# Kernel tuning notes

Measured on AMD Instinct MI355X. Metric: run time of the kernel, lower is better.

Reference implementation:

```python
import jax, jax.numpy as jnp
import numpy as np
import math

B, L, N, DIM, H = 2, 8, 1024, 512, 8
DH = DIM // H

def setup_inputs() -> dict:
    key = jax.random.key(0)
    ks = jax.random.split(key, 9)
    s = 1.0 / math.sqrt(DIM)
    return {
        "x": jax.random.normal(ks[0], (B, L, N, DIM), dtype=jnp.float32),
        "Wq": jax.random.normal(ks[1], (DIM, DIM), dtype=jnp.float32) * s,
        "bq": jnp.zeros((DIM,), dtype=jnp.float32),
        "Wk": jax.random.normal(ks[2], (DIM, DIM), dtype=jnp.float32) * s,
        "bk": jnp.zeros((DIM,), dtype=jnp.float32),
        "Wv": jax.random.normal(ks[3], (DIM, DIM), dtype=jnp.float32) * s,
        "bv": jnp.zeros((DIM,), dtype=jnp.float32),
        "Wo": jax.random.normal(ks[4], (DIM, DIM), dtype=jnp.float32) * s,
        "bo": jnp.zeros((DIM,), dtype=jnp.float32),
    }

def _split_heads(t):
    # 'b l n (h d) -> b l h n d'
    b, l, n, _ = t.shape
    return t.reshape(b, l, n, H, DH).transpose(0, 1, 3, 2, 4)

def reference(x, Wq, bq, Wk, bk, Wv, bv, Wo, bo):
    q = _split_heads(x @ Wq.T + bq)
    # FAITHFUL BUG: source maps (q, v, k) -> (q_mat, k_mat, v_mat),
    # so the "keys" come from the v projection and "values" from the k projection.
    k_mat = _split_heads(x @ Wv.T + bv)
    v_mat = _split_heads(x @ Wk.T + bk)
    # scale is sqrt(Dh * num_heads) = sqrt(dim), as in the source
    scores = jnp.einsum('blhnd,blhmd->blhnm', q, k_mat) / math.sqrt(DIM)
    weights = jax.nn.softmax(scores, axis=-1)
    inter = jnp.einsum('blhnm,blhmd->blhnd', weights, v_mat)
    # 'b l h n d -> b l n (h d)'
    inter = inter.transpose(0, 1, 3, 2, 4).reshape(x.shape[0], x.shape[1], x.shape[2], DIM)
    return inter @ Wo.T + bo
```

## Files before the change

### kernel.cpp

```cpp
#include <hip/hip_runtime.h>
#include <stdint.h>

#define DIMC 512
#define NSEQ 1024
#define BLT  16
#define NHEAD 8
#define DHD  64
#define MTOT (BLT*NSEQ)

typedef float f32x4 __attribute__((ext_vector_type(4)));
typedef short s16x8 __attribute__((ext_vector_type(8)));
typedef short s16x4 __attribute__((ext_vector_type(4)));

__device__ __forceinline__ unsigned short f2bf(float f) {
    unsigned int u = __float_as_uint(f);
    u += 0x7fffu + ((u >> 16) & 1u);
    return (unsigned short)(u >> 16);
}
__device__ __forceinline__ float bf2f(unsigned short h) {
    return __uint_as_float(((unsigned int)h) << 16);
}

#define QSCALE (0.04419417382415922f * 1.4426950408889634f)

__device__ __forceinline__ void gll16(const void* g, void* l) {
    __builtin_amdgcn_global_load_lds(
        (const __attribute__((address_space(1))) void*)g,
        (__attribute__((address_space(3))) void*)l, 16, 0, 0);
}

__device__ __forceinline__ f32x4 mfma16_bf16(s16x4 a, s16x4 b, f32x4 c) {
#if __has_builtin(__builtin_amdgcn_mfma_f32_16x16x16bf16_1k)
    return __builtin_amdgcn_mfma_f32_16x16x16bf16_1k(a, b, c, 0, 0, 0);
#else
    asm volatile("v_mfma_f32_16x16x16_bf16 %0, %1, %2, %0"
                 : "+v"(c) : "v"(a), "v"(b));
    return c;
#endif
}

__device__ __forceinline__ bool detect_bf16(const unsigned short* x) {
    int t = threadIdx.x & 63;
    unsigned short v = x[2 * t];
    int e = (v >> 7) & 0xFF;
    unsigned long long ball = __ballot(e < 100 || e > 137);
    return __popcll(ball) < 16;
}

struct ConvArgs {
    const void* src[9];
    unsigned short* dst[9];
};

__global__ __launch_bounds__(256) void conv_kernel(ConvArgs a,
                                                   const unsigned short* __restrict__ xdet) {
    const bool isbf = detect_bf16(xdet);
    int b = blockIdx.x;
    int seg, idx;
    if (b < 4096)      { seg = 0; idx = (b * 256 + threadIdx.x) * 8; }
    else if (b < 4608) { int t = b - 4096; seg = 1 + (t >> 7);
                         idx = (((t & 127) * 256) + threadIdx.x) * 8; }
    else               { int i = threadIdx.x * 8; seg = 5 + (i >> 9); idx = i & 511; }
    const void* s = a.src[seg];
    unsigned short* d = a.dst[seg];
    if (isbf) {
        *(uint4*)(d + idx) = *(const uint4*)((const unsigned short*)s + idx);
    } else {
        float4 t0 = *(const float4*)((const float*)s + idx);
        float4 t1 = *(const float4*)((const float*)s + idx + 4);
        ushort4 v0{f2bf(t0.x), f2bf(t0.y), f2bf(t0.z), f2bf(t0.w)};
        ushort4 v1{f2bf(t1.x), f2bf(t1.y), f2bf(t1.z), f2bf(t1.w)};
        *(ushort4*)(d + idx)     = v0;
        *(ushort4*)(d + idx + 4) = v1;
    }
}

__device__ __forceinline__ void gemm_core_async(
    const unsigned short* __restrict__ Ap, const unsigned short* __restrict__ Wp,
    int mBase, int nBase, unsigned short* Al, unsigned short* Bl, f32x4 acc[4][4])
{
    const int wave = threadIdx.x >> 6;
    const int lane = threadIdx.x & 63;
    const int lr = lane & 15, lg = lane >> 4;
    const int wm = wave >> 1, wn = wave & 1;
    const int srow = lane >> 3;
    const int scol = (lane & 7) * 8;

    #pragma unroll
    for (int a = 0; a < 4; ++a)
        #pragma unroll
        for (int b = 0; b < 4; ++b) acc[a][b] = (f32x4){0.f, 0.f, 0.f, 0.f};

    for (int k0 = 0; k0 < DIMC; k0 += 64) {
        #pragma unroll
        for (int i = 0; i < 4; ++i) {
            int rbase = (wave * 4 + i) * 8;
            gll16(Ap + (long)(mBase + rbase + srow) * DIMC + k0 + scol, Al + rbase * 64);
            gll16(Wp + (long)(nBase + rbase + srow) * DIMC + k0 + scol, Bl + rbase * 64);
        }
        __syncthreads();

        #pragma unroll
        for (int kk = 0; kk < 64; kk += 32) {
            s16x8 af[4], bf_[4];
            #pragma unroll
            for (int a = 0; a < 4; ++a)
                af[a] = *(const s16x8*)&Al[(wm * 64 + a * 16 + lr) * 64 + kk + lg * 8];
            #pragma unroll
            for (int b = 0; b < 4; ++b)
                bf_[b] = *(const s16x8*)&Bl[(wn * 64 + b * 16 + lr) * 64 + kk + lg * 8];
            #pragma unroll
            for (int a = 0; a < 4; ++a)
                #pragma unroll
                for (int b = 0; b < 4; ++b)
                    acc[a][b] = __builtin_amdgcn_mfma_f32_16x16x32_bf16(af[a], bf_[b], acc[a][b], 0, 0, 0);
        }
        __syncthreads();
    }
}

__global__ __launch_bounds__(256) void proj_kernel(
    const unsigned short* __restrict__ xb,
    const unsigned short* __restrict__ Wqb, const unsigned short* __restrict__ Wkb,
    const unsigned short* __restrict__ Wvb,
    const unsigned short* __restrict__ bqb, const unsigned short* __restrict__ bkb,
    const unsigned short* __restrict__ bvb,
    unsigned short* __restrict__ Q, unsigned short* __restrict__ K,
    unsigned short* __restrict__ Vt)
{
    const int z = blockIdx.z;
    const unsigned short* Wp = (z == 0) ? Wqb : ((z == 1) ? Wvb : Wkb);
    const unsigned short* bp = (z == 0) ? bqb : ((z == 1) ? bvb : bkb);
    unsigned short* outp = (z == 0) ? Q : ((z == 1) ? K : Vt);
    const float oscale = (z == 0) ? QSCALE : 1.0f;

    const int mBase = blockIdx.x * 128;
    const int nBase = blockIdx.y * 128;
    const int lane = threadIdx.x & 63;
    const int lr = lane & 15, lg = lane >> 4;
    const int wm = (threadIdx.x >> 6) >> 1, wn = (threadIdx.x >> 6) & 1;

    __shared__ unsigned short Al[128 * 64];
    __shared__ unsigned short Bl[128 * 64];
    f32x4 acc[4][4];
    gemm_core_async(xb, Wp, mBase, nBase, Al, Bl, acc);

    #pragma unroll
    for (int b = 0; b < 4; ++b) {
        int j = nBase + wn * 64 + b * 16 + lr;
        float bb = bf2f(bp[j]);
        int h = j >> 6, d = j & 63;
        #pragma unroll
        for (int a = 0; a < 4; ++a) {
            int m0 = mBase + wm * 64 + a * 16 + lg * 4;
            int bl = m0 >> 10, n0 = m0 & 1023;
            if (z == 2) {
                ushort4 pk;
                unsigned short* p = (unsigned short*)&pk;
                #pragma unroll
                for (int r = 0; r < 4; ++r) p[r] = f2bf(acc[a][b][r] + bb);
                *(ushort4*)&outp[(((bl << 3) + h) << 16) + (d << 10) + n0] = pk;
            } else {
                #pragma unroll
                for (int r = 0; r < 4; ++r) {
                    float v = (acc[a][b][r] + bb) * oscale;
                    outp[(((bl << 3) + h) << 16) + ((n0 + r) << 6) + d] = f2bf(v);
                }
            }
        }
    }
}

__global__ __launch_bounds__(256) void out_gemm_kernel(
    const unsigned short* __restrict__ inter, const unsigned short* __restrict__ Wob,
    const unsigned short* __restrict__ bob, void* __restrict__ outp,
    const unsigned short* __restrict__ xdet)
{
    const bool isbf = detect_bf16(xdet);
    const int mBase = blockIdx.x * 128;
    const int nBase = blockIdx.y * 128;
    const int lane = threadIdx.x & 63;
    const int lr = lane & 15, lg = lane >> 4;
    const int wm = (threadIdx.x >> 6) >> 1, wn = (threadIdx.x >> 6) & 1;

    __shared__ unsigned short Al[128 * 64];
    __shared__ unsigned short Bl[128 * 64];
    f32x4 acc[4][4];
    gemm_core_async(inter, Wob, mBase, nBase, Al, Bl, acc);

    #pragma unroll
    for (int b = 0; b < 4; ++b) {
        int j = nBase + wn * 64 + b * 16 + lr;
        float bb = bf2f(bob[j]);
        #pragma unroll
        for (int a = 0; a < 4; ++a) {
            #pragma unroll
            for (int r = 0; r < 4; ++r) {
                long m = mBase + wm * 64 + a * 16 + lg * 4 + r;
                float v = acc[a][b][r] + bb;
                if (isbf) ((unsigned short*)outp)[m * DIMC + j] = f2bf(v);
                else      ((float*)outp)[m * DIMC + j] = v;
            }
        }
    }
}

#define SWZ(row, col) ((row) * 64 + ((col) ^ (((row) & 7) * 8)))

__global__ __launch_bounds__(256) void attn_kernel(
    const unsigned short* __restrict__ Q, const unsigned short* __restrict__ K,
    const unsigned short* __restrict__ Vt, unsigned short* __restrict__ inter)
{
    const int inst = blockIdx.x;
    const int bh = inst >> 4;
    const int qt = inst & 15;
    const int wave = threadIdx.x >> 6;
    const int lane = threadIdx.x & 63;
    const int lr = lane & 15;
    const int lg = lane >> 4;

    const unsigned short* Qb = Q + (long)bh * (NSEQ * DHD);
    const int qrow = qt * 64 + wave * 16 + lr;
    s16x8 qf0 = *(const s16x8*)&Qb[qrow * DHD + lg * 8];
    s16x8 qf1 = *(const s16x8*)&Qb[qrow * DHD + 32 + lg * 8];

    __shared__ unsigned short Kl[64 * 64];
    __shared__ unsigned short Vl[64 * 64];

    f32x4 o[4];
    #pragma unroll
    for (int m = 0; m < 4; ++m) o[m] = (f32x4){0.f, 0.f, 0.f, 0.f};
    float l_acc = 0.f;

    for (int kt = 0; kt < 16; ++kt) {
        const unsigned short* Kb = K + (long)bh * (NSEQ * DHD) + kt * 64 * DHD;
        const unsigned short* Vb = Vt + (long)bh * (NSEQ * DHD) + kt * 64;

        #pragma unroll
        for (int i = 0; i < 2; ++i) {
            int f = threadIdx.x + 256 * i;
            int row = f >> 3, c8 = (f & 7) * 8;
            *(uint4*)&Kl[SWZ(row, c8)] = *(const uint4*)&Kb[row * DHD + c8];
            *(uint4*)&Vl[SWZ(row, c8)] = *(const uint4*)&Vb[row * NSEQ + c8];
        }
        __syncthreads();

        f32x4 s[4];
        #pragma unroll
        for (int c = 0; c < 4; ++c) s[c] = (f32x4){0.f, 0.f, 0.f, 0.f};
        #pragma unroll
        for (int kk = 0; kk < 2; ++kk) {
            s16x8 qf = kk ? qf1 : qf0;
            #pragma unroll
            for (int c = 0; c < 4; ++c) {
                s16x8 a = *(const s16x8*)&Kl[SWZ(c * 16 + lr, kk * 32 + lg * 8)];
                s[c] = __builtin_amdgcn_mfma_f32_16x16x32_bf16(a, qf, s[c], 0, 0, 0);
            }
        }

        s16x4 pb[4];
        #pragma unroll
        for (int c = 0; c < 4; ++c) {
            float p0 = __builtin_exp2f(s[c][0]);
            float p1 = __builtin_exp2f(s[c][1]);
            float p2 = __builtin_exp2f(s[c][2]);
            float p3 = __builtin_exp2f(s[c][3]);
            l_acc += (p0 + p1) + (p2 + p3);
            unsigned int u0 = __float_as_uint(p0) + 0x8000u;
            unsigned int u1 = __float_as_uint(p1) + 0x8000u;
            unsigned int u2 = __float_as_uint(p2) + 0x8000u;
            unsigned int u3 = __float_as_uint(p3) + 0x8000u;
            union { s16x4 v; unsigned int u[2]; } pk;
            pk.u[0] = __builtin_amdgcn_perm(u1, u0, 0x07060302u);
            pk.u[1] = __builtin_amdgcn_perm(u3, u2, 0x07060302u);
            pb[c] = pk.v;
        }

        #pragma unroll
        for (int c = 0; c < 4; ++c)
            #pragma unroll
            for (int m = 0; m < 4; ++m) {
                s16x4 a = *(const s16x4*)&Vl[SWZ(m * 16 + lr, c * 16 + lg * 4)];
                o[m] = mfma16_bf16(a, pb[c], o[m]);
            }
        __syncthreads();
    }

    l_acc += __shfl_xor(l_acc, 16);
    l_acc += __shfl_xor(l_acc, 32);
    float inv = 1.f / l_acc;

    const int bl = bh >> 3, h = bh & 7;
    const int n = qt * 64 + wave * 16 + lr;
    #pragma unroll
    for (int m = 0; m < 4; ++m) {
        ushort4 pk;
        unsigned short* p = (unsigned short*)&pk;
        #pragma unroll
        for (int r = 0; r < 4; ++r) p[r] = f2bf(o[m][r] * inv);
        *(ushort4*)&inter[((long)(bl * NSEQ + n)) * DIMC + h * 64 + m * 16 + lg * 4] = pk;
    }
}

extern "C" void kernel_launch(void* const* d_in, const int* in_sizes, int n_in,
                              void* d_out, int out_size, void* d_ws, size_t ws_size,
                              hipStream_t stream) {
    const void* x  = d_in[0];
    const void* Wq = d_in[1]; const void* bq = d_in[2];
    const void* Wk = d_in[3]; const void* bk = d_in[4];
    const void* Wv = d_in[5]; const void* bv = d_in[6];
    const void* Wo = d_in[7]; const void* bo = d_in[8];

    char* ws = (char*)d_ws;
    unsigned short* xb  = (unsigned short*)ws;
    unsigned short* Q   = xb + (long)MTOT * DIMC;
    unsigned short* K   = Q  + (long)MTOT * DIMC;
    unsigned short* Vt  = K  + (long)MTOT * DIMC;
    unsigned short* Wqb = Vt + (long)MTOT * DIMC;
    unsigned short* Wkb = Wqb + DIMC * DIMC;
    unsigned short* Wvb = Wkb + DIMC * DIMC;
    unsigned short* Wob = Wvb + DIMC * DIMC;
    unsigned short* bqb = Wob + DIMC * DIMC;
    unsigned short* bkb = bqb + DIMC;
    unsigned short* bvb = bkb + DIMC;
    unsigned short* bob = bvb + DIMC;

    ConvArgs ca;
    ca.src[0] = x;  ca.src[1] = Wq; ca.src[2] = Wk; ca.src[3] = Wv; ca.src[4] = Wo;
    ca.src[5] = bq; ca.src[6] = bk; ca.src[7] = bv; ca.src[8] = bo;
    ca.dst[0] = xb;  ca.dst[1] = Wqb; ca.dst[2] = Wkb; ca.dst[3] = Wvb; ca.dst[4] = Wob;
    ca.dst[5] = bqb; ca.dst[6] = bkb; ca.dst[7] = bvb; ca.dst[8] = bob;
    conv_kernel<<<4609, 256, 0, stream>>>(ca, (const unsigned short*)x);

    dim3 gp(MTOT / 128, DIMC / 128, 3);
    proj_kernel<<<gp, 256, 0, stream>>>(xb, Wqb, Wkb, Wvb, bqb, bkb, bvb, Q, K, Vt);

    attn_kernel<<<BLT * NHEAD * 16, 256, 0, stream>>>(Q, K, Vt, xb );

    dim3 go(MTOT / 128, DIMC / 128);
    out_gemm_kernel<<<go, 256, 0, stream>>>(xb , Wob, bob, d_out,
                                            (const unsigned short*)x);
}
```

Measured before the change: 248.4 us.

## Process four query tiles per wave in attention to reuse K/V tiles

Each attention block now covers 256 query rows instead of 64. Each wave holds four 16-row query groups and reuses every K and V fragment read from shared memory across all four groups. This cuts global K/V loads and LDS reads per query by a factor of four, and the grid shrinks from 2048 to 512 blocks. In exchange, register pressure rises sharply (64 accumulator vectors plus 64 score vectors per thread), which may lower occupancy or cause spills, and fewer blocks may underfill the GPU.

```diff
diff --git a/kernel.cpp b/kernel.cpp
--- a/kernel.cpp
+++ b/kernel.cpp
@@ -212,25 +212,32 @@
     const unsigned short* __restrict__ Vt, unsigned short* __restrict__ inter)
 {
     const int inst = blockIdx.x;
-    const int bh = inst >> 4;
-    const int qt = inst & 15;
+    const int bh = inst >> 2;
+    const int qt = inst & 3;
     const int wave = threadIdx.x >> 6;
     const int lane = threadIdx.x & 63;
     const int lr = lane & 15;
     const int lg = lane >> 4;
 
     const unsigned short* Qb = Q + (long)bh * (NSEQ * DHD);
-    const int qrow = qt * 64 + wave * 16 + lr;
-    s16x8 qf0 = *(const s16x8*)&Qb[qrow * DHD + lg * 8];
-    s16x8 qf1 = *(const s16x8*)&Qb[qrow * DHD + 32 + lg * 8];
+    const int qbase = qt * 256 + wave * 64;
+
+    s16x8 qf[4][2];
+    #pragma unroll
+    for (int g = 0; g < 4; ++g)
+        #pragma unroll
+        for (int kk = 0; kk < 2; ++kk)
+            qf[g][kk] = *(const s16x8*)&Qb[(qbase + g * 16 + lr) * DHD + kk * 32 + lg * 8];
 
     __shared__ unsigned short Kl[64 * 64];
     __shared__ unsigned short Vl[64 * 64];
 
-    f32x4 o[4];
-    #pragma unroll
-    for (int m = 0; m < 4; ++m) o[m] = (f32x4){0.f, 0.f, 0.f, 0.f};
-    float l_acc = 0.f;
+    f32x4 o[4][4];
+    #pragma unroll
+    for (int g = 0; g < 4; ++g)
+        #pragma unroll
+        for (int m = 0; m < 4; ++m) o[g][m] = (f32x4){0.f, 0.f, 0.f, 0.f};
+    float l_acc[4] = {0.f, 0.f, 0.f, 0.f};
 
     for (int kt = 0; kt < 16; ++kt) {
         const unsigned short* Kb = K + (long)bh * (NSEQ * DHD) + kt * 64 * DHD;
@@ -245,60 +252,75 @@
         }
         __syncthreads();
 
-        f32x4 s[4];
-        #pragma unroll
-        for (int c = 0; c < 4; ++c) s[c] = (f32x4){0.f, 0.f, 0.f, 0.f};
+        f32x4 s[4][4];
+        #pragma unroll
+        for (int g = 0; g < 4; ++g)
+            #pragma unroll
+            for (int c = 0; c < 4; ++c) s[g][c] = (f32x4){0.f, 0.f, 0.f, 0.f};
         #pragma unroll
         for (int kk = 0; kk < 2; ++kk) {
-            s16x8 qf = kk ? qf1 : qf0;
+            s16x8 af[4];
+            #pragma unroll
+            for (int c = 0; c < 4; ++c)
+                af[c] = *(const s16x8*)&Kl[SWZ(c * 16 + lr, kk * 32 + lg * 8)];
+            #pragma unroll
+            for (int g = 0; g < 4; ++g)
+                #pragma unroll
+                for (int c = 0; c < 4; ++c)
+                    s[g][c] = __builtin_amdgcn_mfma_f32_16x16x32_bf16(af[c], qf[g][kk], s[g][c], 0, 0, 0);
+        }
+
+        s16x4 pb[4][4];
+        #pragma unroll
+        for (int g = 0; g < 4; ++g)
             #pragma unroll
             for (int c = 0; c < 4; ++c) {
-                s16x8 a = *(const s16x8*)&Kl[SWZ(c * 16 + lr, kk * 32 + lg * 8)];
-                s[c] = __builtin_amdgcn_mfma_f32_16x16x32_bf16(a, qf, s[c], 0, 0, 0);
+                float p0 = __builtin_exp2f(s[g][c][0]);
+                float p1 = __builtin_exp2f(s[g][c][1]);
+                float p2 = __builtin_exp2f(s[g][c][2]);
+                float p3 = __builtin_exp2f(s[g][c][3]);
+                l_acc[g] += (p0 + p1) + (p2 + p3);
+                unsigned int u0 = __float_as_uint(p0) + 0x8000u;
+                unsigned int u1 = __float_as_uint(p1) + 0x8000u;
+                unsigned int u2 = __float_as_uint(p2) + 0x8000u;
+                unsigned int u3 = __float_as_uint(p3) + 0x8000u;
+                union { s16x4 v; unsigned int u[2]; } pk;
+                pk.u[0] = __builtin_amdgcn_perm(u1, u0, 0x07060302u);
+                pk.u[1] = __builtin_amdgcn_perm(u3, u2, 0x07060302u);
+                pb[g][c] = pk.v;
             }
-        }
-
-        s16x4 pb[4];
+
         #pragma unroll
         for (int c = 0; c < 4; ++c) {
-            float p0 = __builtin_exp2f(s[c][0]);
-            float p1 = __builtin_exp2f(s[c][1]);
-            float p2 = __builtin_exp2f(s[c][2]);
-            float p3 = __builtin_exp2f(s[c][3]);
-            l_acc += (p0 + p1) + (p2 + p3);
-            unsigned int u0 = __float_as_uint(p0) + 0x8000u;
-            unsigned int u1 = __float_as_uint(p1) + 0x8000u;
-            unsigned int u2 = __float_as_uint(p2) + 0x8000u;
-            unsigned int u3 = __float_as_uint(p3) + 0x8000u;
-            union { s16x4 v; unsigned int u[2]; } pk;
-            pk.u[0] = __builtin_amdgcn_perm(u1, u0, 0x07060302u);
-            pk.u[1] = __builtin_amdgcn_perm(u3, u2, 0x07060302u);
-            pb[c] = pk.v;
-        }
-
-        #pragma unroll
-        for (int c = 0; c < 4; ++c)
-            #pragma unroll
-            for (int m = 0; m < 4; ++m) {
-                s16x4 a = *(const s16x4*)&Vl[SWZ(m * 16 + lr, c * 16 + lg * 4)];
-                o[m] = mfma16_bf16(a, pb[c], o[m]);
-            }
+            s16x4 va[4];
+            #pragma unroll
+            for (int m = 0; m < 4; ++m)
+                va[m] = *(const s16x4*)&Vl[SWZ(m * 16 + lr, c * 16 + lg * 4)];
+            #pragma unroll
+            for (int g = 0; g < 4; ++g)
+                #pragma unroll
+                for (int m = 0; m < 4; ++m)
+                    o[g][m] = mfma16_bf16(va[m], pb[g][c], o[g][m]);
+        }
         __syncthreads();
     }
 
-    l_acc += __shfl_xor(l_acc, 16);
-    l_acc += __shfl_xor(l_acc, 32);
-    float inv = 1.f / l_acc;
-
     const int bl = bh >> 3, h = bh & 7;
-    const int n = qt * 64 + wave * 16 + lr;
-    #pragma unroll
-    for (int m = 0; m < 4; ++m) {
-        ushort4 pk;
-        unsigned short* p = (unsigned short*)&pk;
-        #pragma unroll
-        for (int r = 0; r < 4; ++r) p[r] = f2bf(o[m][r] * inv);
-        *(ushort4*)&inter[((long)(bl * NSEQ + n)) * DIMC + h * 64 + m * 16 + lg * 4] = pk;
+    #pragma unroll
+    for (int g = 0; g < 4; ++g) {
+        float l = l_acc[g];
+        l += __shfl_xor(l, 16);
+        l += __shfl_xor(l, 32);
+        float inv = 1.f / l;
+        const int n = qbase + g * 16 + lr;
+        #pragma unroll
+        for (int m = 0; m < 4; ++m) {
+            ushort4 pk;
+            unsigned short* p = (unsigned short*)&pk;
+            #pragma unroll
+            for (int r = 0; r < 4; ++r) p[r] = f2bf(o[g][m][r] * inv);
+            *(ushort4*)&inter[((long)(bl * NSEQ + n)) * DIMC + h * 64 + m * 16 + lg * 4] = pk;
+        }
     }
 }
 
@@ -335,7 +357,7 @@
     dim3 gp(MTOT / 128, DIMC / 128, 3);
     proj_kernel<<<gp, 256, 0, stream>>>(xb, Wqb, Wkb, Wvb, bqb, bkb, bvb, Q, K, Vt);
 
-    attn_kernel<<<BLT * NHEAD * 16, 256, 0, stream>>>(Q, K, Vt, xb );
+    attn_kernel<<<BLT * NHEAD * 4, 256, 0, stream>>>(Q, K, Vt, xb );
 
     dim3 go(MTOT / 128, DIMC / 128);
     out_gemm_kernel<<<go, 256, 0, stream>>>(xb , Wob, bob, d_out,
```

Measured after the change: 241.6 us. 1.03x faster.
